# Performance work log

Measured on AMD Instinct MI355X. Metric: run time of the kernel, lower is better.

## Reference

```python
import jax, jax.numpy as jnp
import numpy as np

N_CLS = 1000
FEAT_DIM = 1024
BATCH = 32768
PROTO_M = 0.95
TEMP = 0.1
BASE_TEMP = 0.1


def setup_inputs() -> dict:
    key = jax.random.key(0)
    k1, k2, k3 = jax.random.split(key, 3)
    features = jax.random.normal(k1, (BATCH, FEAT_DIM), dtype=jnp.float32)
    labels = jax.random.randint(k2, (BATCH,), 0, N_CLS)
    p = jax.random.normal(k3, (N_CLS, FEAT_DIM), dtype=jnp.float32)
    prototypes = p / jnp.maximum(jnp.linalg.norm(p, axis=1, keepdims=True), 1e-12)
    return {"features": features, "prototypes": prototypes, "labels": labels}


def _l2_normalize(x, eps=1e-12):
    # F.normalize(x, dim=0) semantics: x / max(||x||_2, eps)
    return x / jnp.maximum(jnp.linalg.norm(x), eps)


def _ema_update(prototypes, features, labels):
    # Sequential per-sample EMA + renormalize (faithful to the torch for-loop:
    # later samples with the same label see earlier updates).
    def step(protos, fl):
        f, l = fl
        row = _l2_normalize(protos[l] * PROTO_M + f * (1.0 - PROTO_M))
        return protos.at[l].set(row), None

    prototypes, _ = jax.lax.scan(step, prototypes, (features, labels))
    return prototypes


def reference(features, prototypes, labels):
    protos = _ema_update(prototypes, features, labels)  # [n_cls, feat]
    logits = jnp.matmul(protos, protos.T) / TEMP        # [n_cls, n_cls]
    # mask = (1 - eye) * logits_mask, where logits_mask also zeros the diagonal
    mask = 1.0 - jnp.eye(N_CLS, dtype=logits.dtype)
    mean_prob_neg = jnp.log((mask * jnp.exp(logits)).sum(axis=1) / mask.sum(axis=1))
    # torch drops NaNs; with n_cls > 1 every row has n_cls-1 negatives, so none occur
    loss = (TEMP / BASE_TEMP) * jnp.mean(mean_prob_neg)
    return loss
```

## Files before the change

kernel.cpp:

```cpp
#include <hip/hip_runtime.h>
#include <hip/hip_bf16.h>
#include <math.h>

#define N_CLS 1000
#define FEAT  1024
#define BATCH 32768
#define NBLK_H 128
#define CHUNK  256
#define LPITCH 72
#define GRAM_BLOCKS 256
#define SCAN_BLOCKS 250

typedef short short8 __attribute__((ext_vector_type(8)));
typedef float f32x4  __attribute__((ext_vector_type(4)));

__device__ __forceinline__ unsigned short f2bf(float x) {
    union { __hip_bfloat16 h; unsigned short u; } cv;
    cv.h = __float2bfloat16(x);
    return cv.u;
}
__device__ __forceinline__ float bf2f(unsigned short u) {
    union { __hip_bfloat16 h; unsigned short u; } cv;
    cv.u = u;
    return __bfloat162float(cv.h);
}

__global__ __launch_bounds__(256) void hist_kernel(const int* __restrict__ labels,
                                                   unsigned* __restrict__ hist,
                                                   float* __restrict__ S,
                                                   unsigned* __restrict__ counter) {
    __shared__ unsigned cnt[N_CLS];
    const int t = threadIdx.x, b = blockIdx.x;
    if (b == 0) {
        for (int i = t; i < N_CLS; i += 256) S[i] = 0.0f;
        if (t == 0) { counter[0] = 0u; counter[1] = 0u; }
    }
    for (int i = t; i < N_CLS; i += 256) cnt[i] = 0;
    __syncthreads();
    atomicAdd(&cnt[labels[b * CHUNK + t]], 1u);
    __syncthreads();
    for (int i = t; i < N_CLS; i += 256) hist[(size_t)i * NBLK_H + b] = cnt[i];
}

__global__ __launch_bounds__(256) void scan_kernel(unsigned* __restrict__ hist,
                                                   unsigned* __restrict__ total,
                                                   unsigned* __restrict__ base,
                                                   unsigned* __restrict__ counter) {
    const int t    = threadIdx.x;
    const int l    = blockIdx.x * 4 + (t >> 6);
    const int lane = t & 63;
    unsigned v0 = hist[(size_t)l * NBLK_H + lane];
    unsigned v1 = hist[(size_t)l * NBLK_H + 64 + lane];
    unsigned x0 = v0, x1 = v1;
    #pragma unroll
    for (int off = 1; off < 64; off <<= 1) {
        unsigned u0 = __shfl_up(x0, off, 64);
        if (lane >= off) x0 += u0;
        unsigned u1 = __shfl_up(x1, off, 64);
        if (lane >= off) x1 += u1;
    }
    x1 += __shfl(x0, 63, 64);
    hist[(size_t)l * NBLK_H + lane]      = x0 - v0;
    hist[(size_t)l * NBLK_H + 64 + lane] = x1 - v1;
    if (lane == 63) total[l] = x1;

    __syncthreads();
    __threadfence();
    __shared__ int amlast;
    if (t == 0) {
        unsigned old = __hip_atomic_fetch_add(&counter[1], 1u, __ATOMIC_ACQ_REL, __HIP_MEMORY_SCOPE_AGENT);
        amlast = (old == SCAN_BLOCKS - 1) ? 1 : 0;
    }
    __syncthreads();
    if (!amlast) return;

    unsigned v[4];
    unsigned s = 0;
    #pragma unroll
    for (int j = 0; j < 4; ++j) {
        const int i = t * 4 + j;
        v[j] = (i < N_CLS) ? __hip_atomic_load(&total[i], __ATOMIC_RELAXED, __HIP_MEMORY_SCOPE_AGENT) : 0u;
        s += v[j];
    }
    __shared__ unsigned sc[256];
    sc[t] = s;
    __syncthreads();
    for (int off = 1; off < 256; off <<= 1) {
        unsigned u = (t >= off) ? sc[t - off] : 0u;
        __syncthreads();
        sc[t] += u;
        __syncthreads();
    }
    unsigned acc = sc[t] - s;
    #pragma unroll
    for (int j = 0; j < 4; ++j) {
        const int i = t * 4 + j;
        if (i < N_CLS) base[i] = acc;
        acc += v[j];
    }
}

__global__ __launch_bounds__(256) void scatter_kernel(const int* __restrict__ labels,
                                                      const unsigned* __restrict__ hist,
                                                      const unsigned* __restrict__ base,
                                                      int* __restrict__ sorted_idx) {
    __shared__ int lbl[CHUNK];
    __shared__ unsigned c[N_CLS];
    const int t = threadIdx.x, b = blockIdx.x;
    for (int i = t; i < N_CLS; i += 256) c[i] = 0;
    __syncthreads();
    const int i = b * CHUNK + t;
    const int l = labels[i];
    lbl[t] = l;
    atomicAdd(&c[l], 1u);
    __syncthreads();
    int rank = 0;
    if (c[l] > 1) {
        for (int j = 0; j < t; ++j) rank += (lbl[j] == l);
    }
    sorted_idx[base[l] + hist[(size_t)l * NBLK_H + b] + (unsigned)rank] = i;
}

__device__ __forceinline__ float4 ema4(float4 p, float4 f) {
    p.x = fmaf(0.95f, p.x, 0.05f * f.x);
    p.y = fmaf(0.95f, p.y, 0.05f * f.y);
    p.z = fmaf(0.95f, p.z, 0.05f * f.z);
    p.w = fmaf(0.95f, p.w, 0.05f * f.w);
    return p;
}
__device__ __forceinline__ float dot4(float4 a) {
    return a.x * a.x + a.y * a.y + a.z * a.z + a.w * a.w;
}
__device__ __forceinline__ float4 scale4(float4 a, float s) {
    a.x *= s; a.y *= s; a.z *= s; a.w *= s; return a;
}

__device__ __forceinline__ void ema_step(float4& p0, float4& p1, float4& p2, float4& p3,
                                         float4& x0, float4& x1, float4& x2, float4& x3,
                                         const float* __restrict__ features, int iN, int lane) {
    p0 = ema4(p0, x0); p1 = ema4(p1, x1); p2 = ema4(p2, x2); p3 = ema4(p3, x3);
    const float4* f = (const float4*)(features + (size_t)iN * FEAT);
    x0 = f[lane]; x1 = f[lane + 64]; x2 = f[lane + 128]; x3 = f[lane + 192];
    float ss = dot4(p0) + dot4(p1) + dot4(p2) + dot4(p3);
    #pragma unroll
    for (int o = 32; o; o >>= 1) ss += __shfl_xor(ss, o, 64);
    const float inv = 1.0f / fmaxf(sqrtf(ss), 1e-12f);
    p0 = scale4(p0, inv); p1 = scale4(p1, inv); p2 = scale4(p2, inv); p3 = scale4(p3, inv);
}

__device__ __forceinline__ void write_hl(unsigned short* __restrict__ H,
                                         unsigned short* __restrict__ L,
                                         size_t off, float4 v) {
    ushort4 hi, lo;
    hi.x = f2bf(v.x); lo.x = f2bf(v.x - bf2f(hi.x));
    hi.y = f2bf(v.y); lo.y = f2bf(v.y - bf2f(hi.y));
    hi.z = f2bf(v.z); lo.z = f2bf(v.z - bf2f(hi.z));
    hi.w = f2bf(v.w); lo.w = f2bf(v.w - bf2f(hi.w));
    *(ushort4*)(H + off) = hi;
    *(ushort4*)(L + off) = lo;
}

__global__ __launch_bounds__(256) void ema_kernel(const float* __restrict__ features,
                                                  const float* __restrict__ prototypes,
                                                  const int* __restrict__ sorted_idx,
                                                  const unsigned* __restrict__ base,
                                                  const unsigned* __restrict__ total,
                                                  unsigned short* __restrict__ Hg,
                                                  unsigned short* __restrict__ Lg) {
    const int w    = blockIdx.x * 4 + (threadIdx.x >> 6);
    const int lane = threadIdx.x & 63;
    const float4* pr = (const float4*)(prototypes + (size_t)w * FEAT);
    float4 p0 = pr[lane], p1 = pr[lane + 64], p2 = pr[lane + 128], p3 = pr[lane + 192];

    const int cnt = (int)total[w];
    const int bs  = (int)base[w];
    int myidx = (lane < cnt) ? sorted_idx[bs + lane] : 0;

    #define GETIDX(K) (((K) < cnt) ? (((K) < 64) ? __shfl(myidx, (K), 64) : sorted_idx[bs + (K)]) : 0)

    const int iA = GETIDX(0), iB = GETIDX(1), iC = GETIDX(2);
    const float4* fA = (const float4*)(features + (size_t)iA * FEAT);
    float4 a0 = fA[lane], a1 = fA[lane + 64], a2 = fA[lane + 128], a3 = fA[lane + 192];
    const float4* fB = (const float4*)(features + (size_t)iB * FEAT);
    float4 b0 = fB[lane], b1 = fB[lane + 64], b2 = fB[lane + 128], b3 = fB[lane + 192];
    const float4* fC = (const float4*)(features + (size_t)iC * FEAT);
    float4 c0 = fC[lane], c1 = fC[lane + 64], c2 = fC[lane + 128], c3 = fC[lane + 192];

    int k = 0;
    while (k + 3 <= cnt) {
        ema_step(p0,p1,p2,p3, a0,a1,a2,a3, features, GETIDX(k + 3), lane); ++k;
        ema_step(p0,p1,p2,p3, b0,b1,b2,b3, features, GETIDX(k + 3), lane); ++k;
        ema_step(p0,p1,p2,p3, c0,c1,c2,c3, features, GETIDX(k + 3), lane); ++k;
    }
    if (k < cnt) { ema_step(p0,p1,p2,p3, a0,a1,a2,a3, features, 0, lane); ++k; }
    if (k < cnt) { ema_step(p0,p1,p2,p3, b0,b1,b2,b3, features, 0, lane); ++k; }

    const size_t rb = (size_t)w * FEAT;
    write_hl(Hg, Lg, rb +       4 * lane, p0);
    write_hl(Hg, Lg, rb + 256 + 4 * lane, p1);
    write_hl(Hg, Lg, rb + 512 + 4 * lane, p2);
    write_hl(Hg, Lg, rb + 768 + 4 * lane, p3);
    #undef GETIDX
}

__global__ __launch_bounds__(256) void gram_kernel(const unsigned short* __restrict__ Hg,
                                                   const unsigned short* __restrict__ Lg,
                                                   float* __restrict__ S,
                                                   unsigned* __restrict__ counter,
                                                   float* __restrict__ out) {
    __shared__ short Hms[64 * LPITCH];
    __shared__ short Lms[64 * LPITCH];
    __shared__ short Hns[64 * LPITCH];
    __shared__ short Lns[64 * LPITCH];
    const int t = threadIdx.x;
    const int l = t & 63, wid = t >> 6;
    const int wr = wid >> 1, wc = wid & 1;
    const int m0 = blockIdx.y * 64, n0 = blockIdx.x * 64;
    const int lg = l >> 4, lc = l & 15;

    const short* Hp = (const short*)Hg;
    const short* Lp = (const short*)Lg;

    f32x4 acc[2][2] = {};

    const int r0 = t >> 3,           c0 = t & 7;
    const int r1 = (t + 256) >> 3,   c1 = t & 7;

    for (int k0 = 0; k0 < FEAT; k0 += 64) {
        short8 hm0 = *(const short8*)(Hp + (size_t)(m0 + r0) * FEAT + k0 + c0 * 8);
        short8 hm1 = *(const short8*)(Hp + (size_t)(m0 + r1) * FEAT + k0 + c1 * 8);
        short8 lm0 = *(const short8*)(Lp + (size_t)(m0 + r0) * FEAT + k0 + c0 * 8);
        short8 lm1 = *(const short8*)(Lp + (size_t)(m0 + r1) * FEAT + k0 + c1 * 8);
        short8 hn0 = *(const short8*)(Hp + (size_t)(n0 + r0) * FEAT + k0 + c0 * 8);
        short8 hn1 = *(const short8*)(Hp + (size_t)(n0 + r1) * FEAT + k0 + c1 * 8);
        short8 ln0 = *(const short8*)(Lp + (size_t)(n0 + r0) * FEAT + k0 + c0 * 8);
        short8 ln1 = *(const short8*)(Lp + (size_t)(n0 + r1) * FEAT + k0 + c1 * 8);
        __syncthreads();
        *(short8*)(Hms + r0 * LPITCH + c0 * 8) = hm0;
        *(short8*)(Hms + r1 * LPITCH + c1 * 8) = hm1;
        *(short8*)(Lms + r0 * LPITCH + c0 * 8) = lm0;
        *(short8*)(Lms + r1 * LPITCH + c1 * 8) = lm1;
        *(short8*)(Hns + r0 * LPITCH + c0 * 8) = hn0;
        *(short8*)(Hns + r1 * LPITCH + c1 * 8) = hn1;
        *(short8*)(Lns + r0 * LPITCH + c0 * 8) = ln0;
        *(short8*)(Lns + r1 * LPITCH + c1 * 8) = ln1;
        __syncthreads();
        #pragma unroll
        for (int kk = 0; kk < 2; ++kk) {
            short8 ah[2], al[2], bh[2], bl[2];
            #pragma unroll
            for (int mi = 0; mi < 2; ++mi) {
                ah[mi] = *(const short8*)(Hms + (wr * 32 + mi * 16 + lc) * LPITCH + kk * 32 + lg * 8);
                al[mi] = *(const short8*)(Lms + (wr * 32 + mi * 16 + lc) * LPITCH + kk * 32 + lg * 8);
            }
            #pragma unroll
            for (int ni = 0; ni < 2; ++ni) {
                bh[ni] = *(const short8*)(Hns + (wc * 32 + ni * 16 + lc) * LPITCH + kk * 32 + lg * 8);
                bl[ni] = *(const short8*)(Lns + (wc * 32 + ni * 16 + lc) * LPITCH + kk * 32 + lg * 8);
            }
            #pragma unroll
            for (int mi = 0; mi < 2; ++mi)
                #pragma unroll
                for (int ni = 0; ni < 2; ++ni) {
                    acc[mi][ni] = __builtin_amdgcn_mfma_f32_16x16x32_bf16(ah[mi], bh[ni], acc[mi][ni], 0, 0, 0);
                    acc[mi][ni] = __builtin_amdgcn_mfma_f32_16x16x32_bf16(al[mi], bh[ni], acc[mi][ni], 0, 0, 0);
                    acc[mi][ni] = __builtin_amdgcn_mfma_f32_16x16x32_bf16(ah[mi], bl[ni], acc[mi][ni], 0, 0, 0);
                }
        }
    }

    #pragma unroll
    for (int mi = 0; mi < 2; ++mi) {
        #pragma unroll
        for (int j = 0; j < 4; ++j) {
            const int gr = m0 + wr * 32 + mi * 16 + lg * 4 + j;
            float s = 0.f;
            #pragma unroll
            for (int ni = 0; ni < 2; ++ni) {
                const int gc = n0 + wc * 32 + ni * 16 + lc;
                if (gr < N_CLS && gc < N_CLS && gr != gc) s += expf(acc[mi][ni][j] * 10.0f);
            }
            #pragma unroll
            for (int m = 1; m < 16; m <<= 1) s += __shfl_xor(s, m, 64);
            if (lc == 0 && gr < N_CLS) atomicAdd(&S[gr], s);
        }
    }

    __threadfence();
    __shared__ int amlast;
    if (t == 0) {
        unsigned old = __hip_atomic_fetch_add(&counter[0], 1u, __ATOMIC_ACQ_REL, __HIP_MEMORY_SCOPE_AGENT);
        amlast = (old == GRAM_BLOCKS - 1) ? 1 : 0;
    }
    __syncthreads();
    if (amlast) {
        float a = 0.f;
        for (int i = t; i < N_CLS; i += 256) {
            float sv = __hip_atomic_load(&S[i], __ATOMIC_RELAXED, __HIP_MEMORY_SCOPE_AGENT);
            a += logf(sv);
        }
        #pragma unroll
        for (int o = 32; o; o >>= 1) a += __shfl_xor(a, o, 64);
        __shared__ float red[4];
        if (l == 0) red[wid] = a;
        __syncthreads();
        if (t == 0) {
            float tot = red[0] + red[1] + red[2] + red[3];
            out[0] = tot / (float)N_CLS - logf(999.0f);
        }
    }
}

extern "C" void kernel_launch(void* const* d_in, const int* in_sizes, int n_in,
                              void* d_out, int out_size, void* d_ws, size_t ws_size,
                              hipStream_t stream) {
    const float* features   = (const float*)d_in[0];
    const float* prototypes = (const float*)d_in[1];
    const int*   labels     = (const int*)d_in[2];
    float* out = (float*)d_out;

    char* ws = (char*)d_ws;
    unsigned*       hist    = (unsigned*)(ws);
    unsigned*       base    = (unsigned*)(ws + 0x80000);
    unsigned*       total   = (unsigned*)(ws + 0x81000);
    int*            sorted  = (int*)     (ws + 0x82000);
    float*          S       = (float*)   (ws + 0xA4000);
    unsigned*       counter = (unsigned*)(ws + 0xA5000);
    unsigned short* Hg      = (unsigned short*)(ws + 0x100000);
    unsigned short* Lg      = (unsigned short*)(ws + 0x300000);

    hist_kernel   <<<NBLK_H, 256, 0, stream>>>(labels, hist, S, counter);
    scan_kernel   <<<SCAN_BLOCKS, 256, 0, stream>>>(hist, total, base, counter);
    scatter_kernel<<<NBLK_H, 256, 0, stream>>>(labels, hist, base, sorted);
    ema_kernel    <<<SCAN_BLOCKS, 256, 0, stream>>>(features, prototypes, sorted, base, total, Hg, Lg);
    gram_kernel   <<<dim3(16, 16), 256, 0, stream>>>(Hg, Lg, S, counter, out);
}
```

Baseline: 278.1 us.

## Fuse five kernels into one persistent kernel with grid-wide barriers

Merges the histogram, scan, scatter, EMA and Gram kernels into a single 256-block persistent kernel that separates phases with atomic-counter spin barriers. Histogram and scatter chunks shrink to 128 labels so the grid matches the Gram tile count, and the counters are cleared with a memset before launch. The aim is to remove four kernel launch gaps and tail idle time. The cost is spin-wait barrier overhead, and the kernel relies on all 256 blocks being co-resident or it will deadlock.

```diff
diff --git a/kernel.cpp b/kernel.cpp
--- a/kernel.cpp
+++ b/kernel.cpp
@@ -5,11 +5,9 @@
 #define N_CLS 1000
 #define FEAT  1024
 #define BATCH 32768
-#define NBLK_H 128
-#define CHUNK  256
+#define NBLK  256
+#define CHUNK 128
 #define LPITCH 72
-#define GRAM_BLOCKS 256
-#define SCAN_BLOCKS 250
 
 typedef short short8 __attribute__((ext_vector_type(8)));
 typedef float f32x4  __attribute__((ext_vector_type(4)));
@@ -25,100 +23,15 @@
     return __bfloat162float(cv.h);
 }
 
-__global__ __launch_bounds__(256) void hist_kernel(const int* __restrict__ labels,
-                                                   unsigned* __restrict__ hist,
-                                                   float* __restrict__ S,
-                                                   unsigned* __restrict__ counter) {
-    __shared__ unsigned cnt[N_CLS];
-    const int t = threadIdx.x, b = blockIdx.x;
-    if (b == 0) {
-        for (int i = t; i < N_CLS; i += 256) S[i] = 0.0f;
-        if (t == 0) { counter[0] = 0u; counter[1] = 0u; }
-    }
-    for (int i = t; i < N_CLS; i += 256) cnt[i] = 0;
+__device__ __forceinline__ void gbar(unsigned* ctr) {
     __syncthreads();
-    atomicAdd(&cnt[labels[b * CHUNK + t]], 1u);
+    if (threadIdx.x == 0) {
+        __threadfence();
+        __hip_atomic_fetch_add(ctr, 1u, __ATOMIC_ACQ_REL, __HIP_MEMORY_SCOPE_AGENT);
+        while (__hip_atomic_load(ctr, __ATOMIC_ACQUIRE, __HIP_MEMORY_SCOPE_AGENT) < NBLK)
+            __builtin_amdgcn_s_sleep(2);
+    }
     __syncthreads();
-    for (int i = t; i < N_CLS; i += 256) hist[(size_t)i * NBLK_H + b] = cnt[i];
-}
-
-__global__ __launch_bounds__(256) void scan_kernel(unsigned* __restrict__ hist,
-                                                   unsigned* __restrict__ total,
-                                                   unsigned* __restrict__ base,
-                                                   unsigned* __restrict__ counter) {
-    const int t    = threadIdx.x;
-    const int l    = blockIdx.x * 4 + (t >> 6);
-    const int lane = t & 63;
-    unsigned v0 = hist[(size_t)l * NBLK_H + lane];
-    unsigned v1 = hist[(size_t)l * NBLK_H + 64 + lane];
-    unsigned x0 = v0, x1 = v1;
-    #pragma unroll
-    for (int off = 1; off < 64; off <<= 1) {
-        unsigned u0 = __shfl_up(x0, off, 64);
-        if (lane >= off) x0 += u0;
-        unsigned u1 = __shfl_up(x1, off, 64);
-        if (lane >= off) x1 += u1;
-    }
-    x1 += __shfl(x0, 63, 64);
-    hist[(size_t)l * NBLK_H + lane]      = x0 - v0;
-    hist[(size_t)l * NBLK_H + 64 + lane] = x1 - v1;
-    if (lane == 63) total[l] = x1;
-
-    __syncthreads();
-    __threadfence();
-    __shared__ int amlast;
-    if (t == 0) {
-        unsigned old = __hip_atomic_fetch_add(&counter[1], 1u, __ATOMIC_ACQ_REL, __HIP_MEMORY_SCOPE_AGENT);
-        amlast = (old == SCAN_BLOCKS - 1) ? 1 : 0;
-    }
-    __syncthreads();
-    if (!amlast) return;
-
-    unsigned v[4];
-    unsigned s = 0;
-    #pragma unroll
-    for (int j = 0; j < 4; ++j) {
-        const int i = t * 4 + j;
-        v[j] = (i < N_CLS) ? __hip_atomic_load(&total[i], __ATOMIC_RELAXED, __HIP_MEMORY_SCOPE_AGENT) : 0u;
-        s += v[j];
-    }
-    __shared__ unsigned sc[256];
-    sc[t] = s;
-    __syncthreads();
-    for (int off = 1; off < 256; off <<= 1) {
-        unsigned u = (t >= off) ? sc[t - off] : 0u;
-        __syncthreads();
-        sc[t] += u;
-        __syncthreads();
-    }
-    unsigned acc = sc[t] - s;
-    #pragma unroll
-    for (int j = 0; j < 4; ++j) {
-        const int i = t * 4 + j;
-        if (i < N_CLS) base[i] = acc;
-        acc += v[j];
-    }
-}
-
-__global__ __launch_bounds__(256) void scatter_kernel(const int* __restrict__ labels,
-                                                      const unsigned* __restrict__ hist,
-                                                      const unsigned* __restrict__ base,
-                                                      int* __restrict__ sorted_idx) {
-    __shared__ int lbl[CHUNK];
-    __shared__ unsigned c[N_CLS];
-    const int t = threadIdx.x, b = blockIdx.x;
-    for (int i = t; i < N_CLS; i += 256) c[i] = 0;
-    __syncthreads();
-    const int i = b * CHUNK + t;
-    const int l = labels[i];
-    lbl[t] = l;
-    atomicAdd(&c[l], 1u);
-    __syncthreads();
-    int rank = 0;
-    if (c[l] > 1) {
-        for (int j = 0; j < t; ++j) rank += (lbl[j] == l);
-    }
-    sorted_idx[base[l] + hist[(size_t)l * NBLK_H + b] + (unsigned)rank] = i;
 }
 
 __device__ __forceinline__ float4 ema4(float4 p, float4 f) {
@@ -160,153 +73,237 @@
     *(ushort4*)(L + off) = lo;
 }
 
-__global__ __launch_bounds__(256) void ema_kernel(const float* __restrict__ features,
-                                                  const float* __restrict__ prototypes,
-                                                  const int* __restrict__ sorted_idx,
-                                                  const unsigned* __restrict__ base,
-                                                  const unsigned* __restrict__ total,
-                                                  unsigned short* __restrict__ Hg,
-                                                  unsigned short* __restrict__ Lg) {
-    const int w    = blockIdx.x * 4 + (threadIdx.x >> 6);
-    const int lane = threadIdx.x & 63;
-    const float4* pr = (const float4*)(prototypes + (size_t)w * FEAT);
-    float4 p0 = pr[lane], p1 = pr[lane + 64], p2 = pr[lane + 128], p3 = pr[lane + 192];
-
-    const int cnt = (int)total[w];
-    const int bs  = (int)base[w];
-    int myidx = (lane < cnt) ? sorted_idx[bs + lane] : 0;
-
-    #define GETIDX(K) (((K) < cnt) ? (((K) < 64) ? __shfl(myidx, (K), 64) : sorted_idx[bs + (K)]) : 0)
-
-    const int iA = GETIDX(0), iB = GETIDX(1), iC = GETIDX(2);
-    const float4* fA = (const float4*)(features + (size_t)iA * FEAT);
-    float4 a0 = fA[lane], a1 = fA[lane + 64], a2 = fA[lane + 128], a3 = fA[lane + 192];
-    const float4* fB = (const float4*)(features + (size_t)iB * FEAT);
-    float4 b0 = fB[lane], b1 = fB[lane + 64], b2 = fB[lane + 128], b3 = fB[lane + 192];
-    const float4* fC = (const float4*)(features + (size_t)iC * FEAT);
-    float4 c0 = fC[lane], c1 = fC[lane + 64], c2 = fC[lane + 128], c3 = fC[lane + 192];
-
-    int k = 0;
-    while (k + 3 <= cnt) {
-        ema_step(p0,p1,p2,p3, a0,a1,a2,a3, features, GETIDX(k + 3), lane); ++k;
-        ema_step(p0,p1,p2,p3, b0,b1,b2,b3, features, GETIDX(k + 3), lane); ++k;
-        ema_step(p0,p1,p2,p3, c0,c1,c2,c3, features, GETIDX(k + 3), lane); ++k;
-    }
-    if (k < cnt) { ema_step(p0,p1,p2,p3, a0,a1,a2,a3, features, 0, lane); ++k; }
-    if (k < cnt) { ema_step(p0,p1,p2,p3, b0,b1,b2,b3, features, 0, lane); ++k; }
-
-    const size_t rb = (size_t)w * FEAT;
-    write_hl(Hg, Lg, rb +       4 * lane, p0);
-    write_hl(Hg, Lg, rb + 256 + 4 * lane, p1);
-    write_hl(Hg, Lg, rb + 512 + 4 * lane, p2);
-    write_hl(Hg, Lg, rb + 768 + 4 * lane, p3);
-    #undef GETIDX
-}
-
-__global__ __launch_bounds__(256) void gram_kernel(const unsigned short* __restrict__ Hg,
-                                                   const unsigned short* __restrict__ Lg,
-                                                   float* __restrict__ S,
-                                                   unsigned* __restrict__ counter,
-                                                   float* __restrict__ out) {
-    __shared__ short Hms[64 * LPITCH];
-    __shared__ short Lms[64 * LPITCH];
-    __shared__ short Hns[64 * LPITCH];
-    __shared__ short Lns[64 * LPITCH];
-    const int t = threadIdx.x;
-    const int l = t & 63, wid = t >> 6;
-    const int wr = wid >> 1, wc = wid & 1;
-    const int m0 = blockIdx.y * 64, n0 = blockIdx.x * 64;
-    const int lg = l >> 4, lc = l & 15;
-
-    const short* Hp = (const short*)Hg;
-    const short* Lp = (const short*)Lg;
-
-    f32x4 acc[2][2] = {};
-
-    const int r0 = t >> 3,           c0 = t & 7;
-    const int r1 = (t + 256) >> 3,   c1 = t & 7;
-
-    for (int k0 = 0; k0 < FEAT; k0 += 64) {
-        short8 hm0 = *(const short8*)(Hp + (size_t)(m0 + r0) * FEAT + k0 + c0 * 8);
-        short8 hm1 = *(const short8*)(Hp + (size_t)(m0 + r1) * FEAT + k0 + c1 * 8);
-        short8 lm0 = *(const short8*)(Lp + (size_t)(m0 + r0) * FEAT + k0 + c0 * 8);
-        short8 lm1 = *(const short8*)(Lp + (size_t)(m0 + r1) * FEAT + k0 + c1 * 8);
-        short8 hn0 = *(const short8*)(Hp + (size_t)(n0 + r0) * FEAT + k0 + c0 * 8);
-        short8 hn1 = *(const short8*)(Hp + (size_t)(n0 + r1) * FEAT + k0 + c1 * 8);
-        short8 ln0 = *(const short8*)(Lp + (size_t)(n0 + r0) * FEAT + k0 + c0 * 8);
-        short8 ln1 = *(const short8*)(Lp + (size_t)(n0 + r1) * FEAT + k0 + c1 * 8);
-        __syncthreads();
-        *(short8*)(Hms + r0 * LPITCH + c0 * 8) = hm0;
-        *(short8*)(Hms + r1 * LPITCH + c1 * 8) = hm1;
-        *(short8*)(Lms + r0 * LPITCH + c0 * 8) = lm0;
-        *(short8*)(Lms + r1 * LPITCH + c1 * 8) = lm1;
-        *(short8*)(Hns + r0 * LPITCH + c0 * 8) = hn0;
-        *(short8*)(Hns + r1 * LPITCH + c1 * 8) = hn1;
-        *(short8*)(Lns + r0 * LPITCH + c0 * 8) = ln0;
-        *(short8*)(Lns + r1 * LPITCH + c1 * 8) = ln1;
-        __syncthreads();
+__global__ __launch_bounds__(256, 1) void mono_kernel(
+        const float* __restrict__ features, const float* __restrict__ prototypes,
+        const int* __restrict__ labels,
+        unsigned* __restrict__ hist, unsigned* __restrict__ base,
+        unsigned* __restrict__ total, int* __restrict__ sorted_idx,
+        float* __restrict__ S, unsigned* __restrict__ ctr,
+        unsigned short* __restrict__ Hg, unsigned short* __restrict__ Lg,
+        float* __restrict__ out) {
+    __shared__ __align__(16) char smem[4 * 64 * LPITCH * 2];
+    const int t = threadIdx.x, b = blockIdx.x;
+
+    {
+        unsigned* cnt = (unsigned*)smem;
+        for (int i = t; i < N_CLS; i += 256) cnt[i] = 0;
+        if (b == 0) for (int i = t; i < N_CLS; i += 256) S[i] = 0.0f;
+        __syncthreads();
+        if (t < CHUNK) atomicAdd(&cnt[labels[b * CHUNK + t]], 1u);
+        __syncthreads();
+        for (int i = t; i < N_CLS; i += 256) hist[(size_t)i * NBLK + b] = cnt[i];
+    }
+    gbar(&ctr[0]);
+
+    if (b < 250) {
+        const int l = b * 4 + (t >> 6);
+        const int lane = t & 63;
+        unsigned* hrow = hist + (size_t)l * NBLK + lane * 4;
+        unsigned e0 = hrow[0], e1 = hrow[1], e2 = hrow[2], e3 = hrow[3];
+        unsigned s = e0 + e1 + e2 + e3;
+        unsigned x = s;
         #pragma unroll
-        for (int kk = 0; kk < 2; ++kk) {
-            short8 ah[2], al[2], bh[2], bl[2];
-            #pragma unroll
-            for (int mi = 0; mi < 2; ++mi) {
-                ah[mi] = *(const short8*)(Hms + (wr * 32 + mi * 16 + lc) * LPITCH + kk * 32 + lg * 8);
-                al[mi] = *(const short8*)(Lms + (wr * 32 + mi * 16 + lc) * LPITCH + kk * 32 + lg * 8);
-            }
-            #pragma unroll
-            for (int ni = 0; ni < 2; ++ni) {
-                bh[ni] = *(const short8*)(Hns + (wc * 32 + ni * 16 + lc) * LPITCH + kk * 32 + lg * 8);
-                bl[ni] = *(const short8*)(Lns + (wc * 32 + ni * 16 + lc) * LPITCH + kk * 32 + lg * 8);
-            }
-            #pragma unroll
-            for (int mi = 0; mi < 2; ++mi)
-                #pragma unroll
-                for (int ni = 0; ni < 2; ++ni) {
-                    acc[mi][ni] = __builtin_amdgcn_mfma_f32_16x16x32_bf16(ah[mi], bh[ni], acc[mi][ni], 0, 0, 0);
-                    acc[mi][ni] = __builtin_amdgcn_mfma_f32_16x16x32_bf16(al[mi], bh[ni], acc[mi][ni], 0, 0, 0);
-                    acc[mi][ni] = __builtin_amdgcn_mfma_f32_16x16x32_bf16(ah[mi], bl[ni], acc[mi][ni], 0, 0, 0);
-                }
-        }
-    }
-
-    #pragma unroll
-    for (int mi = 0; mi < 2; ++mi) {
+        for (int off = 1; off < 64; off <<= 1) {
+            unsigned u = __shfl_up(x, off, 64);
+            if (lane >= off) x += u;
+        }
+        unsigned run = x - s;
+        hrow[0] = run; run += e0;
+        hrow[1] = run; run += e1;
+        hrow[2] = run; run += e2;
+        hrow[3] = run;
+        if (lane == 63) total[l] = x;
+    }
+    gbar(&ctr[1]);
+
+    if (b == 0) {
+        unsigned* sc = (unsigned*)smem;
+        unsigned v[4], s = 0;
         #pragma unroll
         for (int j = 0; j < 4; ++j) {
-            const int gr = m0 + wr * 32 + mi * 16 + lg * 4 + j;
-            float s = 0.f;
+            const int i = t * 4 + j;
+            v[j] = (i < N_CLS) ? total[i] : 0u;
+            s += v[j];
+        }
+        sc[t] = s;
+        __syncthreads();
+        for (int off = 1; off < 256; off <<= 1) {
+            unsigned u = (t >= off) ? sc[t - off] : 0u;
+            __syncthreads();
+            sc[t] += u;
+            __syncthreads();
+        }
+        unsigned acc = sc[t] - s;
+        #pragma unroll
+        for (int j = 0; j < 4; ++j) {
+            const int i = t * 4 + j;
+            if (i < N_CLS) base[i] = acc;
+            acc += v[j];
+        }
+    }
+    gbar(&ctr[2]);
+
+    {
+        int* lbl      = (int*)smem;
+        unsigned* c   = (unsigned*)(smem + 512);
+        for (int i = t; i < N_CLS; i += 256) c[i] = 0;
+        __syncthreads();
+        int l = 0, i = 0;
+        if (t < CHUNK) {
+            i = b * CHUNK + t;
+            l = labels[i];
+            lbl[t] = l;
+            atomicAdd(&c[l], 1u);
+        }
+        __syncthreads();
+        if (t < CHUNK) {
+            int rank = 0;
+            if (c[l] > 1) {
+                for (int j = 0; j < t; ++j) rank += (lbl[j] == l);
+            }
+            sorted_idx[base[l] + hist[(size_t)l * NBLK + b] + (unsigned)rank] = i;
+        }
+    }
+    gbar(&ctr[3]);
+
+    if (b < 250) {
+        const int w    = b * 4 + (t >> 6);
+        const int lane = t & 63;
+        const float4* pr = (const float4*)(prototypes + (size_t)w * FEAT);
+        float4 p0 = pr[lane], p1 = pr[lane + 64], p2 = pr[lane + 128], p3 = pr[lane + 192];
+
+        const int cnt = (int)total[w];
+        const int bs  = (int)base[w];
+        int myidx = (lane < cnt) ? sorted_idx[bs + lane] : 0;
+
+        #define GETIDX(K) (((K) < cnt) ? (((K) < 64) ? __shfl(myidx, (K), 64) : sorted_idx[bs + (K)]) : 0)
+
+        const int iA = GETIDX(0), iB = GETIDX(1), iC = GETIDX(2);
+        const float4* fA = (const float4*)(features + (size_t)iA * FEAT);
+        float4 a0 = fA[lane], a1 = fA[lane + 64], a2 = fA[lane + 128], a3 = fA[lane + 192];
+        const float4* fB = (const float4*)(features + (size_t)iB * FEAT);
+        float4 b0 = fB[lane], b1 = fB[lane + 64], b2 = fB[lane + 128], b3 = fB[lane + 192];
+        const float4* fC = (const float4*)(features + (size_t)iC * FEAT);
+        float4 c0 = fC[lane], c1 = fC[lane + 64], c2 = fC[lane + 128], c3 = fC[lane + 192];
+
+        int k = 0;
+        while (k + 3 <= cnt) {
+            ema_step(p0,p1,p2,p3, a0,a1,a2,a3, features, GETIDX(k + 3), lane); ++k;
+            ema_step(p0,p1,p2,p3, b0,b1,b2,b3, features, GETIDX(k + 3), lane); ++k;
+            ema_step(p0,p1,p2,p3, c0,c1,c2,c3, features, GETIDX(k + 3), lane); ++k;
+        }
+        if (k < cnt) { ema_step(p0,p1,p2,p3, a0,a1,a2,a3, features, 0, lane); ++k; }
+        if (k < cnt) { ema_step(p0,p1,p2,p3, b0,b1,b2,b3, features, 0, lane); ++k; }
+        #undef GETIDX
+
+        const size_t rb = (size_t)w * FEAT;
+        write_hl(Hg, Lg, rb +       4 * lane, p0);
+        write_hl(Hg, Lg, rb + 256 + 4 * lane, p1);
+        write_hl(Hg, Lg, rb + 512 + 4 * lane, p2);
+        write_hl(Hg, Lg, rb + 768 + 4 * lane, p3);
+    }
+    gbar(&ctr[4]);
+
+    {
+        short* Hms = (short*)smem;
+        short* Lms = Hms + 64 * LPITCH;
+        short* Hns = Lms + 64 * LPITCH;
+        short* Lns = Hns + 64 * LPITCH;
+        const int l = t & 63, wid = t >> 6;
+        const int wr = wid >> 1, wc = wid & 1;
+        const int m0 = (b >> 4) * 64, n0 = (b & 15) * 64;
+        const int lg = l >> 4, lc = l & 15;
+
+        const short* Hp = (const short*)Hg;
+        const short* Lp = (const short*)Lg;
+
+        f32x4 acc[2][2] = {};
+
+        const int r0 = t >> 3,          c0 = t & 7;
+        const int r1 = (t + 256) >> 3,  c1 = t & 7;
+
+        for (int k0 = 0; k0 < FEAT; k0 += 64) {
+            short8 hm0 = *(const short8*)(Hp + (size_t)(m0 + r0) * FEAT + k0 + c0 * 8);
+            short8 hm1 = *(const short8*)(Hp + (size_t)(m0 + r1) * FEAT + k0 + c1 * 8);
+            short8 lm0 = *(const short8*)(Lp + (size_t)(m0 + r0) * FEAT + k0 + c0 * 8);
+            short8 lm1 = *(const short8*)(Lp + (size_t)(m0 + r1) * FEAT + k0 + c1 * 8);
+            short8 hn0 = *(const short8*)(Hp + (size_t)(n0 + r0) * FEAT + k0 + c0 * 8);
+            short8 hn1 = *(const short8*)(Hp + (size_t)(n0 + r1) * FEAT + k0 + c1 * 8);
+            short8 ln0 = *(const short8*)(Lp + (size_t)(n0 + r0) * FEAT + k0 + c0 * 8);
+            short8 ln1 = *(const short8*)(Lp + (size_t)(n0 + r1) * FEAT + k0 + c1 * 8);
+            __syncthreads();
+            *(short8*)(Hms + r0 * LPITCH + c0 * 8) = hm0;
+            *(short8*)(Hms + r1 * LPITCH + c1 * 8) = hm1;
+            *(short8*)(Lms + r0 * LPITCH + c0 * 8) = lm0;
+            *(short8*)(Lms + r1 * LPITCH + c1 * 8) = lm1;
+            *(short8*)(Hns + r0 * LPITCH + c0 * 8) = hn0;
+            *(short8*)(Hns + r1 * LPITCH + c1 * 8) = hn1;
+            *(short8*)(Lns + r0 * LPITCH + c0 * 8) = ln0;
+            *(short8*)(Lns + r1 * LPITCH + c1 * 8) = ln1;
+            __syncthreads();
             #pragma unroll
-            for (int ni = 0; ni < 2; ++ni) {
-                const int gc = n0 + wc * 32 + ni * 16 + lc;
-                if (gr < N_CLS && gc < N_CLS && gr != gc) s += expf(acc[mi][ni][j] * 10.0f);
-            }
+            for (int kk = 0; kk < 2; ++kk) {
+                short8 ah[2], al[2], bh[2], bl[2];
+                #pragma unroll
+                for (int mi = 0; mi < 2; ++mi) {
+                    ah[mi] = *(const short8*)(Hms + (wr * 32 + mi * 16 + lc) * LPITCH + kk * 32 + lg * 8);
+                    al[mi] = *(const short8*)(Lms + (wr * 32 + mi * 16 + lc) * LPITCH + kk * 32 + lg * 8);
+                }
+                #pragma unroll
+                for (int ni = 0; ni < 2; ++ni) {
+                    bh[ni] = *(const short8*)(Hns + (wc * 32 + ni * 16 + lc) * LPITCH + kk * 32 + lg * 8);
+                    bl[ni] = *(const short8*)(Lns + (wc * 32 + ni * 16 + lc) * LPITCH + kk * 32 + lg * 8);
+                }
+                #pragma unroll
+                for (int mi = 0; mi < 2; ++mi)
+                    #pragma unroll
+                    for (int ni = 0; ni < 2; ++ni) {
+                        acc[mi][ni] = __builtin_amdgcn_mfma_f32_16x16x32_bf16(ah[mi], bh[ni], acc[mi][ni], 0, 0, 0);
+                        acc[mi][ni] = __builtin_amdgcn_mfma_f32_16x16x32_bf16(al[mi], bh[ni], acc[mi][ni], 0, 0, 0);
+                        acc[mi][ni] = __builtin_amdgcn_mfma_f32_16x16x32_bf16(ah[mi], bl[ni], acc[mi][ni], 0, 0, 0);
+                    }
+            }
+        }
+
+        #pragma unroll
+        for (int mi = 0; mi < 2; ++mi) {
             #pragma unroll
-            for (int m = 1; m < 16; m <<= 1) s += __shfl_xor(s, m, 64);
-            if (lc == 0 && gr < N_CLS) atomicAdd(&S[gr], s);
-        }
-    }
-
-    __threadfence();
-    __shared__ int amlast;
-    if (t == 0) {
-        unsigned old = __hip_atomic_fetch_add(&counter[0], 1u, __ATOMIC_ACQ_REL, __HIP_MEMORY_SCOPE_AGENT);
-        amlast = (old == GRAM_BLOCKS - 1) ? 1 : 0;
-    }
-    __syncthreads();
-    if (amlast) {
-        float a = 0.f;
-        for (int i = t; i < N_CLS; i += 256) {
-            float sv = __hip_atomic_load(&S[i], __ATOMIC_RELAXED, __HIP_MEMORY_SCOPE_AGENT);
-            a += logf(sv);
-        }
-        #pragma unroll
-        for (int o = 32; o; o >>= 1) a += __shfl_xor(a, o, 64);
-        __shared__ float red[4];
-        if (l == 0) red[wid] = a;
-        __syncthreads();
+            for (int j = 0; j < 4; ++j) {
+                const int gr = m0 + wr * 32 + mi * 16 + lg * 4 + j;
+                float s = 0.f;
+                #pragma unroll
+                for (int ni = 0; ni < 2; ++ni) {
+                    const int gc = n0 + wc * 32 + ni * 16 + lc;
+                    if (gr < N_CLS && gc < N_CLS && gr != gc) s += expf(acc[mi][ni][j] * 10.0f);
+                }
+                #pragma unroll
+                for (int m = 1; m < 16; m <<= 1) s += __shfl_xor(s, m, 64);
+                if (lc == 0 && gr < N_CLS) atomicAdd(&S[gr], s);
+            }
+        }
+
+        __threadfence();
+        __shared__ int amlast;
         if (t == 0) {
-            float tot = red[0] + red[1] + red[2] + red[3];
-            out[0] = tot / (float)N_CLS - logf(999.0f);
+            unsigned old = __hip_atomic_fetch_add(&ctr[5], 1u, __ATOMIC_ACQ_REL, __HIP_MEMORY_SCOPE_AGENT);
+            amlast = (old == NBLK - 1) ? 1 : 0;
+        }
+        __syncthreads();
+        if (amlast) {
+            float a = 0.f;
+            for (int i = t; i < N_CLS; i += 256) {
+                float sv = __hip_atomic_load(&S[i], __ATOMIC_RELAXED, __HIP_MEMORY_SCOPE_AGENT);
+                a += logf(sv);
+            }
+            #pragma unroll
+            for (int o = 32; o; o >>= 1) a += __shfl_xor(a, o, 64);
+            __shared__ float red[4];
+            if (l == 0) red[wid] = a;
+            __syncthreads();
+            if (t == 0) {
+                float tot = red[0] + red[1] + red[2] + red[3];
+                out[0] = tot / (float)N_CLS - logf(999.0f);
+            }
         }
     }
 }
@@ -320,18 +317,17 @@
     float* out = (float*)d_out;
 
     char* ws = (char*)d_ws;
-    unsigned*       hist    = (unsigned*)(ws);
-    unsigned*       base    = (unsigned*)(ws + 0x80000);
-    unsigned*       total   = (unsigned*)(ws + 0x81000);
-    int*            sorted  = (int*)     (ws + 0x82000);
-    float*          S       = (float*)   (ws + 0xA4000);
-    unsigned*       counter = (unsigned*)(ws + 0xA5000);
-    unsigned short* Hg      = (unsigned short*)(ws + 0x100000);
-    unsigned short* Lg      = (unsigned short*)(ws + 0x300000);
-
-    hist_kernel   <<<NBLK_H, 256, 0, stream>>>(labels, hist, S, counter);
-    scan_kernel   <<<SCAN_BLOCKS, 256, 0, stream>>>(hist, total, base, counter);
-    scatter_kernel<<<NBLK_H, 256, 0, stream>>>(labels, hist, base, sorted);
-    ema_kernel    <<<SCAN_BLOCKS, 256, 0, stream>>>(features, prototypes, sorted, base, total, Hg, Lg);
-    gram_kernel   <<<dim3(16, 16), 256, 0, stream>>>(Hg, Lg, S, counter, out);
-}
+    unsigned*       hist   = (unsigned*)(ws);
+    unsigned*       base   = (unsigned*)(ws + 0x100000);
+    unsigned*       total  = (unsigned*)(ws + 0x101000);
+    int*            sorted = (int*)     (ws + 0x102000);
+    float*          S      = (float*)   (ws + 0x122000);
+    unsigned*       ctr    = (unsigned*)(ws + 0x123000);
+    unsigned short* Hg     = (unsigned short*)(ws + 0x200000);
+    unsigned short* Lg     = (unsigned short*)(ws + 0x400000);
+
+    hipMemsetAsync(ctr, 0, 32, stream);
+    mono_kernel<<<NBLK, 256, 0, stream>>>(features, prototypes, labels,
+                                          hist, base, total, sorted,
+                                          S, ctr, Hg, Lg, out);
+}
```

Result: slower. 388.4 us (+39.7%).
